# Kernel optimization log

Measured on AMD Instinct MI355X. Metric: run time of the kernel, lower is better.

Reference implementation:

```python
import jax, jax.numpy as jnp
import numpy as np

B, NQ, NK, D_EQUI, D_INV, D_MSG, D_FF, D_OUT = 2, 768, 768, 256, 256, 32, 128, 64


def setup_inputs() -> dict:
    key = jax.random.key(0)
    ks = jax.random.split(key, 14)
    s = 0.05  # weight init scale
    inp = {
        'q_equi': jax.random.normal(ks[0], (B, NQ, 3, D_EQUI), dtype=jnp.float32),
        'q_inv': jax.random.normal(ks[1], (B, NQ, D_INV), dtype=jnp.float32),
        'k_equi': jax.random.normal(ks[2], (B, NK, 3, D_EQUI), dtype=jnp.float32),
        'k_inv': jax.random.normal(ks[3], (B, NK, D_INV), dtype=jnp.float32),
        # projection params (stored [in, out]; torch Linear is [out, in])
        'Wqi': jax.random.normal(ks[4], (D_INV, D_MSG), dtype=jnp.float32) * s,
        'bqi': jnp.zeros((D_MSG,), jnp.float32),
        'Wki': jax.random.normal(ks[5], (D_INV, D_MSG), dtype=jnp.float32) * s,
        'bki': jnp.zeros((D_MSG,), jnp.float32),
        'Wqe': jax.random.normal(ks[6], (D_EQUI, D_MSG), dtype=jnp.float32) * s,
        'bqe': jnp.zeros((D_MSG,), jnp.float32),
        'Wke': jax.random.normal(ks[7], (D_EQUI, D_MSG), dtype=jnp.float32) * s,
        'bke': jnp.zeros((D_MSG,), jnp.float32),
        # message MLP: in_feats = 4*d_message (q_inv, k_inv, dotprods, dists)
        'W1': jax.random.normal(ks[8], (4 * D_MSG, D_FF), dtype=jnp.float32) * s,
        'b1': jnp.zeros((D_FF,), jnp.float32),
        'W2': jax.random.normal(ks[9], (D_FF, D_OUT), dtype=jnp.float32) * s,
        'b2': jnp.zeros((D_OUT,), jnp.float32),
    }
    return inp


def reference(q_equi, q_inv, k_equi, k_inv, Wqi, bqi, Wki, bki, Wqe, bqe, Wke, bke, W1, b1, W2, b2):
    b, nq = q_inv.shape[0], q_inv.shape[1]
    nk = k_inv.shape[1]
    # invariant projections -> [B, N, m]
    qi = q_inv @ Wqi + bqi
    ki = k_inv @ Wki + bki
    # equivariant projections -> [B, N, 3, m]
    qe = q_equi @ Wqe + bqe
    ke = k_equi @ Wke + bke
    # pairwise dot products over the 3D coordinate axis -> [B, Nq, Nk, m]
    dotprods = jnp.einsum('bqcm,bkcm->bqkm', qe, ke)
    # pairwise vector distances -> [B, Nq, Nk, m]
    vec = qe[:, :, None, :, :] - ke[:, None, :, :, :]  # [B, Nq, Nk, 3, m]
    dists = jnp.sqrt(jnp.sum(vec * vec, axis=3))
    feats = jnp.concatenate([
        jnp.broadcast_to(qi[:, :, None, :], (b, nq, nk, qi.shape[-1])),
        jnp.broadcast_to(ki[:, None, :, :], (b, nq, nk, ki.shape[-1])),
        dotprods,
        dists,
    ], axis=-1)  # [B, Nq, Nk, 4m]
    h = jax.nn.silu(feats @ W1 + b1)
    return h @ W2 + b2  # [B, Nq, Nk, d_out]
```

## Files before the change

kernel.cpp:

```cpp
#include <hip/hip_runtime.h>
#include <cstdint>

#define B_    2
#define NQ_   768
#define NK_   768
#define DE_   256
#define DI_   256
#define DM_   32
#define FF_   128
#define DO_   64
#define NB_   4

typedef float    f32x4  __attribute__((ext_vector_type(4)));
typedef _Float16 half8  __attribute__((ext_vector_type(8)));
typedef _Float16 half2v __attribute__((ext_vector_type(2)));

__global__ __launch_bounds__(256) void node_pre_all(
    const float* __restrict__ q_inv, const float* __restrict__ q_equi,
    const float* __restrict__ k_inv, const float* __restrict__ k_equi,
    const float* __restrict__ Wqi, const float* __restrict__ bqi,
    const float* __restrict__ Wki, const float* __restrict__ bki,
    const float* __restrict__ Wqe, const float* __restrict__ bqe,
    const float* __restrict__ Wke, const float* __restrict__ bke,
    const float* __restrict__ W1,  const float* __restrict__ b1,
    const float* __restrict__ W2,
    float* __restrict__ qe, float* __restrict__ qq, float* __restrict__ Aq,
    float* __restrict__ ke, float* __restrict__ kk, float* __restrict__ Bk,
    _Float16* __restrict__ pk)
{
  const int side = blockIdx.y;
  const int t = threadIdx.x;

  if (blockIdx.x == (B_*NQ_)/NB_) {
    if (side == 0) {
      for (int i = t; i < 8192; i += 256) {
        const int j = i & 7, ln = (i>>3)&63, s = (i>>9)&1, nt = i>>10;
        const int row = 64 + s*32 + (ln>>4)*8 + j, col = nt*16 + (ln&15);
        pk[i] = (_Float16)W1[row*FF_ + col];
      }
    } else {
      for (int i = t; i < 8192; i += 256) {
        const int j = i & 7, ln = (i>>3)&63, s = (i>>9)&3, nt = i>>11;
        const int row = s*32 + (ln>>4)*8 + j, col = nt*16 + (ln&15);
        pk[8192 + i] = (_Float16)W2[row*DO_ + col];
      }
    }
    return;
  }

  const float* inv  = side ? k_inv  : q_inv;
  const float* equi = side ? k_equi : q_equi;
  const float* Wi   = side ? Wki : Wqi;
  const float* bi   = side ? bki : bqi;
  const float* We   = side ? Wke : Wqe;
  const float* be   = side ? bke : bqe;
  const int w1RowOff = side ? 32 : 0;
  const int addB1    = side ? 0 : 1;
  float* e_out  = side ? ke : qe;
  float* sq_out = side ? kk : qq;
  float* ab_out = side ? Bk : Aq;

  __shared__ __align__(16) float W_s[DE_*DM_];
  __shared__ __align__(16) float eq_s[NB_*3*DE_];
  __shared__ __align__(16) float inv_s[NB_*DI_];
  __shared__ float e_s[NB_*96];
  __shared__ float qi_s[NB_*DM_];

  const int node0 = blockIdx.x * NB_;

  { const f32x4* g = (const f32x4*)(equi + (size_t)node0*3*DE_);
    f32x4* d = (f32x4*)eq_s;
    #pragma unroll
    for (int i = 0; i < 3; ++i) d[t + 256*i] = g[t + 256*i]; }
  { const f32x4* g = (const f32x4*)(inv + (size_t)node0*DI_);
    ((f32x4*)inv_s)[t] = g[t]; }
  { const f32x4* g = (const f32x4*)We;
    f32x4* d = (f32x4*)W_s;
    #pragma unroll
    for (int i = 0; i < 8; ++i) d[t + 256*i] = g[t + 256*i]; }
  __syncthreads();

  auto dotW = [&](const float* __restrict__ x, const int m) -> float {
    float a0 = 0.f, a1 = 0.f, a2 = 0.f, a3 = 0.f;
    #pragma unroll 16
    for (int d = 0; d < 256; d += 4) {
      a0 = fmaf(x[d+0], W_s[(d+0)*DM_ + m], a0);
      a1 = fmaf(x[d+1], W_s[(d+1)*DM_ + m], a1);
      a2 = fmaf(x[d+2], W_s[(d+2)*DM_ + m], a2);
      a3 = fmaf(x[d+3], W_s[(d+3)*DM_ + m], a3);
    }
    return (a0+a1)+(a2+a3);
  };

  { const int node = t>>6, c = (t>>5)&1, m = t&31;
    const float v = be[m] + dotW(eq_s + node*3*DE_ + c*DE_, m);
    e_s[node*96 + c*32 + m] = v;
    e_out[(size_t)(node0+node)*96 + c*32 + m] = v; }
  if (t < 128) {
    const int node = t>>5, m = t&31;
    const float v = be[m] + dotW(eq_s + node*3*DE_ + 2*DE_, m);
    e_s[node*96 + 64 + m] = v;
    e_out[(size_t)(node0+node)*96 + 64 + m] = v; }
  __syncthreads();

  { const f32x4* g = (const f32x4*)Wi;
    f32x4* d = (f32x4*)W_s;
    #pragma unroll
    for (int i = 0; i < 8; ++i) d[t + 256*i] = g[t + 256*i]; }
  if (t < NB_*32) {
    const int node = t>>5, m = t&31;
    const float v0 = e_s[node*96+m], v1 = e_s[node*96+32+m], v2 = e_s[node*96+64+m];
    sq_out[(size_t)(node0+node)*32 + m] = v0*v0 + v1*v1 + v2*v2; }
  __syncthreads();

  if (t < NB_*32) {
    const int node = t>>5, m = t&31;
    qi_s[node*32 + m] = bi[m] + dotW(inv_s + node*DI_, m); }
  __syncthreads();

  #pragma unroll
  for (int oo = 0; oo < 2; ++oo) {
    const int o = t + oo*256;
    const int node = o>>7, f = o&127;
    float acc = addB1 ? b1[f] : 0.f;
    #pragma unroll
    for (int m = 0; m < DM_; ++m)
      acc = fmaf(qi_s[node*32 + m], W1[(w1RowOff+m)*FF_ + f], acc);
    ab_out[(size_t)(node0+node)*FF_ + f] = acc;
  }
}

__global__ __launch_bounds__(256, 4) void pair_main(
    const float* __restrict__ qe_g, const float* __restrict__ ke_g,
    const float* __restrict__ qq_g, const float* __restrict__ kk_g,
    const float* __restrict__ Aq_g, const float* __restrict__ Bk_g,
    const _Float16* __restrict__ pk, const float* __restrict__ b2,
    float* __restrict__ out)
{
  __shared__ __align__(16) float qe_s[8*100];
  __shared__ __align__(16) float ke_s[16*100];
  __shared__ __align__(16) float qq_s[8*36];
  __shared__ __align__(16) float kk_s[16*36];
  __shared__ __align__(16) float A_s[8*132];
  __shared__ __align__(16) float B_s[16*132];
  __shared__ __align__(16) _Float16 h_t[4][16*72];

  const int tid = threadIdx.x;
  const int b  = blockIdx.z;
  const int q0 = blockIdx.y * 8;
  const int k0 = blockIdx.x * 16;

  { const f32x4* p = (const f32x4*)(qe_g + ((size_t)b*NQ_ + q0)*96);
    if (tid < 192) ((f32x4*)qe_s)[(tid/24)*25 + tid%24] = p[tid]; }
  { const f32x4* p = (const f32x4*)(ke_g + ((size_t)b*NK_ + k0)*96);
    for (int i = tid; i < 384; i += 256) ((f32x4*)ke_s)[(i/24)*25 + i%24] = p[i]; }
  { const f32x4* p = (const f32x4*)(qq_g + ((size_t)b*NQ_ + q0)*32);
    if (tid < 64) ((f32x4*)qq_s)[(tid>>3)*9 + (tid&7)] = p[tid]; }
  { const f32x4* p = (const f32x4*)(kk_g + ((size_t)b*NK_ + k0)*32);
    if (tid < 128) ((f32x4*)kk_s)[(tid>>3)*9 + (tid&7)] = p[tid]; }
  { const f32x4* p = (const f32x4*)(Aq_g + ((size_t)b*NQ_ + q0)*128);
    ((f32x4*)A_s)[(tid>>5)*33 + (tid&31)] = p[tid]; }
  { const f32x4* p = (const f32x4*)(Bk_g + ((size_t)b*NK_ + k0)*128);
    for (int i = tid; i < 512; i += 256) ((f32x4*)B_s)[(i>>5)*33 + (i&31)] = p[i]; }
  __syncthreads();

  const int lane = tid & 63;
  const int w    = tid >> 6;
  const int n15  = lane & 15;
  const int quad = lane >> 4;
  const int mq   = quad * 8;

  const half8* pk1 = (const half8*)pk;
  const half8* pk2 = (const half8*)(pk + 8192);
  _Float16* hrow = &h_t[w][n15*72];

  f32x4 acc2[2][4];
  #pragma unroll
  for (int t = 0; t < 2; ++t)
    #pragma unroll
    for (int nt = 0; nt < 4; ++nt)
      acc2[t][nt] = (f32x4){0.f,0.f,0.f,0.f};

  #pragma unroll
  for (int t = 0; t < 2; ++t) {
    const int qL = 2*w + t;

    half8 A0, A1;
    #pragma unroll
    for (int hh = 0; hh < 2; ++hh) {
      const int mo = mq + hh*4;
      const f32x4 qe0 = *(const f32x4*)&qe_s[qL*100 +      mo];
      const f32x4 qe1 = *(const f32x4*)&qe_s[qL*100 + 32 + mo];
      const f32x4 qe2 = *(const f32x4*)&qe_s[qL*100 + 64 + mo];
      const f32x4 ke0 = *(const f32x4*)&ke_s[n15*100 +      mo];
      const f32x4 ke1 = *(const f32x4*)&ke_s[n15*100 + 32 + mo];
      const f32x4 ke2 = *(const f32x4*)&ke_s[n15*100 + 64 + mo];
      const f32x4 qqv = *(const f32x4*)&qq_s[qL*36 + mo];
      const f32x4 kkv = *(const f32x4*)&kk_s[n15*36 + mo];
      #pragma unroll
      for (int e = 0; e < 4; ++e) {
        float d = qe0[e]*ke0[e];
        d = fmaf(qe1[e], ke1[e], d);
        d = fmaf(qe2[e], ke2[e], d);
        A0[hh*4+e] = (_Float16)d;
        float v = qqv[e] + kkv[e] - 2.f*d;
        v = fmaxf(v, 0.f);
        A1[hh*4+e] = (_Float16)__builtin_sqrtf(v);
      }
    }

    #pragma unroll
    for (int ch = 0; ch < 2; ++ch) {
      f32x4 acc1[4];
      #pragma unroll
      for (int nt = 0; nt < 4; ++nt) acc1[nt] = (f32x4){0.f,0.f,0.f,0.f};
      {
        half8 Bs[4];
        #pragma unroll
        for (int nt = 0; nt < 4; ++nt) Bs[nt] = pk1[(((ch*4+nt)*2 + 0)<<6) + lane];
        #pragma unroll
        for (int nt = 0; nt < 4; ++nt)
          acc1[nt] = __builtin_amdgcn_mfma_f32_16x16x32_f16(Bs[nt], A0, acc1[nt], 0, 0, 0);
        #pragma unroll
        for (int nt = 0; nt < 4; ++nt) Bs[nt] = pk1[(((ch*4+nt)*2 + 1)<<6) + lane];
        #pragma unroll
        for (int nt = 0; nt < 4; ++nt)
          acc1[nt] = __builtin_amdgcn_mfma_f32_16x16x32_f16(Bs[nt], A1, acc1[nt], 0, 0, 0);
      }

      #pragma unroll
      for (int ntl = 0; ntl < 4; ++ntl) {
        const int nt = ch*4 + ntl;
        const f32x4 Af = *(const f32x4*)&A_s[qL*132 + nt*16 + quad*4];
        const f32x4 Bf = *(const f32x4*)&B_s[n15*132 + nt*16 + quad*4];
        _Float16 hv[4];
        #pragma unroll
        for (int r = 0; r < 4; ++r) {
          const float x = acc1[ntl][r] + Af[r] + Bf[r];
          const float e = __builtin_amdgcn_exp2f(-1.44269504f * x);
          hv[r] = (_Float16)(x * __builtin_amdgcn_rcpf(1.f + e));
        }
        half2v p0; p0[0] = hv[0]; p0[1] = hv[1];
        half2v p1; p1[0] = hv[2]; p1[1] = hv[3];
        *(half2v*)&hrow[ntl*16 + quad*4 + 0] = p0;
        *(half2v*)&hrow[ntl*16 + quad*4 + 2] = p1;
      }

      #pragma unroll
      for (int sl = 0; sl < 2; ++sl) {
        const half8 Hf = *(const half8*)&hrow[sl*32 + mq];
        const int s = ch*2 + sl;
        half8 B2s[4];
        #pragma unroll
        for (int nt = 0; nt < 4; ++nt) B2s[nt] = pk2[((nt*4 + s)<<6) + lane];
        #pragma unroll
        for (int nt = 0; nt < 4; ++nt)
          acc2[t][nt] = __builtin_amdgcn_mfma_f32_16x16x32_f16(B2s[nt], Hf, acc2[t][nt], 0, 0, 0);
      }
    }
  }

  f32x4 bias[4];
  #pragma unroll
  for (int nt = 0; nt < 4; ++nt) bias[nt] = *(const f32x4*)&b2[nt*16 + quad*4];
  const size_t outBase = (((size_t)b*NQ_ + q0)*NK_ + k0)*DO_;
  #pragma unroll
  for (int t = 0; t < 2; ++t) {
    const int qL = 2*w + t;
    float* orow = out + outBase + ((size_t)qL*NK_ + n15)*DO_;
    #pragma unroll
    for (int nt = 0; nt < 4; ++nt) {
      const f32x4 v = acc2[t][nt] + bias[nt];
      *(f32x4*)&orow[nt*16 + quad*4] = v;
    }
  }
}

extern "C" void kernel_launch(void* const* d_in, const int* in_sizes, int n_in,
                              void* d_out, int out_size, void* d_ws, size_t ws_size,
                              hipStream_t stream) {
  const float* q_equi = (const float*)d_in[0];
  const float* q_inv  = (const float*)d_in[1];
  const float* k_equi = (const float*)d_in[2];
  const float* k_inv  = (const float*)d_in[3];
  const float* Wqi = (const float*)d_in[4];
  const float* bqi = (const float*)d_in[5];
  const float* Wki = (const float*)d_in[6];
  const float* bki = (const float*)d_in[7];
  const float* Wqe = (const float*)d_in[8];
  const float* bqe = (const float*)d_in[9];
  const float* Wke = (const float*)d_in[10];
  const float* bke = (const float*)d_in[11];
  const float* W1  = (const float*)d_in[12];
  const float* b1  = (const float*)d_in[13];
  const float* W2  = (const float*)d_in[14];
  const float* b2  = (const float*)d_in[15];

  float* ws = (float*)d_ws;
  float* qe = ws;
  float* ke = qe + (size_t)B_*NQ_*96;
  float* qq = ke + (size_t)B_*NK_*96;
  float* kk = qq + (size_t)B_*NQ_*32;
  float* Aq = kk + (size_t)B_*NK_*32;
  float* Bk = Aq + (size_t)B_*NQ_*128;
  _Float16* pk = (_Float16*)(Bk + (size_t)B_*NK_*128);

  dim3 ngrid(B_*NQ_/NB_ + 1, 2);
  node_pre_all<<<ngrid, 256, 0, stream>>>(
      q_inv, q_equi, k_inv, k_equi, Wqi, bqi, Wki, bki, Wqe, bqe, Wke, bke,
      W1, b1, W2, qe, qq, Aq, ke, kk, Bk, pk);

  dim3 grid(NK_/16, NQ_/8, B_);
  pair_main<<<grid, 256, 0, stream>>>(qe, ke, qq, kk, Aq, Bk, pk, b2, (float*)d_out);
}
```

Baseline: 418.6 us.

## Stage packed MLP weights in LDS and reuse them across both query rows

Each block now copies the packed fp16 W1/W2 fragments (32 KB) into shared memory at launch. It also swaps the loop order so each weight fragment is loaded once per chunk and reused for both query rows, and the B-bias fragments are hoisted likewise. The launch-bounds occupancy hint is dropped and h stores are widened to half4. The aim is to cut repeated global/L2 weight fetches per wave. The cost is more LDS per block, a larger per-block prologue copy, and higher register pressure from holding 16 weight fragments, which may lower occupancy.

```diff
diff --git a/kernel.cpp b/kernel.cpp
--- a/kernel.cpp
+++ b/kernel.cpp
@@ -13,7 +13,7 @@
 
 typedef float    f32x4  __attribute__((ext_vector_type(4)));
 typedef _Float16 half8  __attribute__((ext_vector_type(8)));
-typedef _Float16 half2v __attribute__((ext_vector_type(2)));
+typedef _Float16 half4  __attribute__((ext_vector_type(4)));
 
 __global__ __launch_bounds__(256) void node_pre_all(
     const float* __restrict__ q_inv, const float* __restrict__ q_equi,
@@ -130,7 +130,7 @@
   }
 }
 
-__global__ __launch_bounds__(256, 4) void pair_main(
+__global__ __launch_bounds__(256) void pair_main(
     const float* __restrict__ qe_g, const float* __restrict__ ke_g,
     const float* __restrict__ qq_g, const float* __restrict__ kk_g,
     const float* __restrict__ Aq_g, const float* __restrict__ Bk_g,
@@ -144,12 +144,17 @@
   __shared__ __align__(16) float A_s[8*132];
   __shared__ __align__(16) float B_s[16*132];
   __shared__ __align__(16) _Float16 h_t[4][16*72];
+  __shared__ __align__(16) _Float16 pk_s[16384];
 
   const int tid = threadIdx.x;
   const int b  = blockIdx.z;
   const int q0 = blockIdx.y * 8;
   const int k0 = blockIdx.x * 16;
 
+  { const f32x4* p = (const f32x4*)pk;
+    f32x4* d = (f32x4*)pk_s;
+    #pragma unroll
+    for (int i = 0; i < 8; ++i) d[tid + 256*i] = p[tid + 256*i]; }
   { const f32x4* p = (const f32x4*)(qe_g + ((size_t)b*NQ_ + q0)*96);
     if (tid < 192) ((f32x4*)qe_s)[(tid/24)*25 + tid%24] = p[tid]; }
   { const f32x4* p = (const f32x4*)(ke_g + ((size_t)b*NK_ + k0)*96);
@@ -170,22 +175,14 @@
   const int quad = lane >> 4;
   const int mq   = quad * 8;
 
-  const half8* pk1 = (const half8*)pk;
-  const half8* pk2 = (const half8*)(pk + 8192);
+  const half8* pk1 = (const half8*)pk_s;
+  const half8* pk2 = (const half8*)(pk_s + 8192);
   _Float16* hrow = &h_t[w][n15*72];
 
-  f32x4 acc2[2][4];
-  #pragma unroll
-  for (int t = 0; t < 2; ++t)
-    #pragma unroll
-    for (int nt = 0; nt < 4; ++nt)
-      acc2[t][nt] = (f32x4){0.f,0.f,0.f,0.f};
-
+  half8 A0[2], A1[2];
   #pragma unroll
   for (int t = 0; t < 2; ++t) {
     const int qL = 2*w + t;
-
-    half8 A0, A1;
     #pragma unroll
     for (int hh = 0; hh < 2; ++hh) {
       const int mo = mq + hh*4;
@@ -202,61 +199,71 @@
         float d = qe0[e]*ke0[e];
         d = fmaf(qe1[e], ke1[e], d);
         d = fmaf(qe2[e], ke2[e], d);
-        A0[hh*4+e] = (_Float16)d;
-        float v = qqv[e] + kkv[e] - 2.f*d;
+        A0[t][hh*4+e] = (_Float16)d;
+        float v = fmaf(-2.f, d, qqv[e] + kkv[e]);
         v = fmaxf(v, 0.f);
-        A1[hh*4+e] = (_Float16)__builtin_sqrtf(v);
+        A1[t][hh*4+e] = (_Float16)__builtin_sqrtf(v);
       }
     }
-
-    #pragma unroll
-    for (int ch = 0; ch < 2; ++ch) {
+  }
+
+  f32x4 acc2[2][4];
+  #pragma unroll
+  for (int t = 0; t < 2; ++t)
+    #pragma unroll
+    for (int nt = 0; nt < 4; ++nt)
+      acc2[t][nt] = (f32x4){0.f,0.f,0.f,0.f};
+
+  #pragma unroll
+  for (int ch = 0; ch < 2; ++ch) {
+    half8 B1a[4], B1b[4], B2a[4], B2b[4];
+    #pragma unroll
+    for (int nt = 0; nt < 4; ++nt) {
+      B1a[nt] = pk1[(((ch*4+nt)*2 + 0)<<6) + lane];
+      B1b[nt] = pk1[(((ch*4+nt)*2 + 1)<<6) + lane];
+      B2a[nt] = pk2[((nt*4 + 2*ch + 0)<<6) + lane];
+      B2b[nt] = pk2[((nt*4 + 2*ch + 1)<<6) + lane];
+    }
+    f32x4 Bf[4];
+    #pragma unroll
+    for (int ntl = 0; ntl < 4; ++ntl)
+      Bf[ntl] = *(const f32x4*)&B_s[n15*132 + (ch*4+ntl)*16 + quad*4];
+
+    #pragma unroll
+    for (int t = 0; t < 2; ++t) {
+      const int qL = 2*w + t;
+
       f32x4 acc1[4];
       #pragma unroll
       for (int nt = 0; nt < 4; ++nt) acc1[nt] = (f32x4){0.f,0.f,0.f,0.f};
-      {
-        half8 Bs[4];
-        #pragma unroll
-        for (int nt = 0; nt < 4; ++nt) Bs[nt] = pk1[(((ch*4+nt)*2 + 0)<<6) + lane];
-        #pragma unroll
-        for (int nt = 0; nt < 4; ++nt)
-          acc1[nt] = __builtin_amdgcn_mfma_f32_16x16x32_f16(Bs[nt], A0, acc1[nt], 0, 0, 0);
-        #pragma unroll
-        for (int nt = 0; nt < 4; ++nt) Bs[nt] = pk1[(((ch*4+nt)*2 + 1)<<6) + lane];
-        #pragma unroll
-        for (int nt = 0; nt < 4; ++nt)
-          acc1[nt] = __builtin_amdgcn_mfma_f32_16x16x32_f16(Bs[nt], A1, acc1[nt], 0, 0, 0);
-      }
+      #pragma unroll
+      for (int nt = 0; nt < 4; ++nt)
+        acc1[nt] = __builtin_amdgcn_mfma_f32_16x16x32_f16(B1a[nt], A0[t], acc1[nt], 0, 0, 0);
+      #pragma unroll
+      for (int nt = 0; nt < 4; ++nt)
+        acc1[nt] = __builtin_amdgcn_mfma_f32_16x16x32_f16(B1b[nt], A1[t], acc1[nt], 0, 0, 0);
 
       #pragma unroll
       for (int ntl = 0; ntl < 4; ++ntl) {
-        const int nt = ch*4 + ntl;
-        const f32x4 Af = *(const f32x4*)&A_s[qL*132 + nt*16 + quad*4];
-        const f32x4 Bf = *(const f32x4*)&B_s[n15*132 + nt*16 + quad*4];
-        _Float16 hv[4];
+        const f32x4 Af = *(const f32x4*)&A_s[qL*132 + (ch*4+ntl)*16 + quad*4];
+        half4 hv;
         #pragma unroll
         for (int r = 0; r < 4; ++r) {
-          const float x = acc1[ntl][r] + Af[r] + Bf[r];
+          const float x = acc1[ntl][r] + Af[r] + Bf[ntl][r];
           const float e = __builtin_amdgcn_exp2f(-1.44269504f * x);
           hv[r] = (_Float16)(x * __builtin_amdgcn_rcpf(1.f + e));
         }
-        half2v p0; p0[0] = hv[0]; p0[1] = hv[1];
-        half2v p1; p1[0] = hv[2]; p1[1] = hv[3];
-        *(half2v*)&hrow[ntl*16 + quad*4 + 0] = p0;
-        *(half2v*)&hrow[ntl*16 + quad*4 + 2] = p1;
+        *(half4*)&hrow[ntl*16 + quad*4] = hv;
       }
 
-      #pragma unroll
-      for (int sl = 0; sl < 2; ++sl) {
-        const half8 Hf = *(const half8*)&hrow[sl*32 + mq];
-        const int s = ch*2 + sl;
-        half8 B2s[4];
-        #pragma unroll
-        for (int nt = 0; nt < 4; ++nt) B2s[nt] = pk2[((nt*4 + s)<<6) + lane];
+      { const half8 Hf = *(const half8*)&hrow[0*32 + mq];
         #pragma unroll
         for (int nt = 0; nt < 4; ++nt)
-          acc2[t][nt] = __builtin_amdgcn_mfma_f32_16x16x32_f16(B2s[nt], Hf, acc2[t][nt], 0, 0, 0);
-      }
+          acc2[t][nt] = __builtin_amdgcn_mfma_f32_16x16x32_f16(B2a[nt], Hf, acc2[t][nt], 0, 0, 0); }
+      { const half8 Hf = *(const half8*)&hrow[1*32 + mq];
+        #pragma unroll
+        for (int nt = 0; nt < 4; ++nt)
+          acc2[t][nt] = __builtin_amdgcn_mfma_f32_16x16x32_f16(B2b[nt], Hf, acc2[t][nt], 0, 0, 0); }
     }
   }
 
```

New measurement: 420.3 us. Within noise of the previous version (+0.4%).
